# Kernel optimization log

Hardware: AMD Instinct MI355X
Metric: run time of the kernel (lower is better)

The kernel has to match this reference:

```python
import jax, jax.numpy as jnp
import numpy as np

CS = [32, 32, 64, 128, 256, 256, 128, 96, 96]
NC = 19
N0, N1, N2, N3, N4 = 50000, 20000, 8000, 3200, 1300


def build_shapes():
    cs = CS
    def rb(ci, co):
        t = [(27, ci, co), (27, co, co)]
        if ci != co:
            t.append((ci, co))  # 1x1 shortcut conv
        return t
    s = [(27, 4, cs[0]), (27, cs[0], cs[0])]                       # stem
    s += [(8, cs[0], cs[0])] + rb(cs[0], cs[1]) + rb(cs[1], cs[1])  # stage1
    s += [(8, cs[1], cs[1])] + rb(cs[1], cs[2]) + rb(cs[2], cs[2])  # stage2
    s += [(8, cs[2], cs[2])] + rb(cs[2], cs[3]) + rb(cs[3], cs[3])  # stage3
    s += [(8, cs[3], cs[3])] + rb(cs[3], cs[4]) + rb(cs[4], cs[4])  # stage4
    s += [(8, cs[4], cs[5])] + rb(cs[5] + cs[3], cs[5]) + rb(cs[5], cs[5])  # up1
    s += [(8, cs[5], cs[6])] + rb(cs[6] + cs[2], cs[6]) + rb(cs[6], cs[6])  # up2
    s += [(8, cs[6], cs[7])] + rb(cs[7] + cs[1], cs[7]) + rb(cs[7], cs[7])  # up3
    s += [(8, cs[7], cs[8])] + rb(cs[8] + cs[0], cs[8]) + rb(cs[8], cs[8])  # up4
    s += [(cs[8], NC), (NC,), (cs[8], cs[8]), (cs[8],), (cs[8], 128), (128,)]
    return s

P_TOTAL = sum(int(np.prod(sh)) for sh in build_shapes())


def _bn(x):
    # train-mode BatchNorm, gamma=1 beta=0 (set by weight_initialization)
    return (x - x.mean(0)) * jax.lax.rsqrt(jnp.var(x, 0) + 1e-5)


def _spconv(x, nbr, W):
    # sparse conv as gather-GEMM-scatter over K kernel offsets.
    # x: [Nin, Cin], nbr: [Nout, K] row indices into x, W: [K, Cin, Cout]
    acc0 = jnp.zeros((nbr.shape[0], W.shape[-1]), x.dtype)
    def step(acc, kw):
        idx, Wk = kw
        return acc + x[idx] @ Wk, None
    acc, _ = jax.lax.scan(step, acc0, (nbr.T, W))
    return acc


def _spdeconv(x, parent, off, W):
    # transposed ks=2 stride=2 conv: each fine voxel has exactly one coarse
    # parent and one kernel-offset id. out[i] = x[parent[i]] @ W[off[i]]
    y = jnp.einsum('nc,kcd->nkd', x[parent], W)  # [Nf, 8, Cout]
    return jnp.take_along_axis(y, off[:, None, None], axis=1)[:, 0, :]


def _cbr(x, nbr, W):
    return jax.nn.relu(_bn(_spconv(x, nbr, W)))


def _resblock(x, nbr, take, ci, co):
    w1 = take(); w2 = take()
    h = _bn(_spconv(jax.nn.relu(_bn(_spconv(x, nbr, w1))), nbr, w2))
    s = x if ci == co else _bn(x @ take())
    return jax.nn.relu(h + s)


def _forward(x, nbr0, nbr1, nbr2, nbr3, nbr4, d1, d2, d3, d4,
             u1p, u1o, u2p, u2o, u3p, u3o, u4p, u4o, params):
    parts = []
    o = 0
    for sh in build_shapes():
        n = int(np.prod(sh))
        parts.append(params[o:o + n].reshape(sh))
        o += n
    it = iter(parts)
    take = lambda: next(it)
    cs = CS
    x0 = _cbr(x, nbr0, take()); x0 = _cbr(x0, nbr0, take())            # stem
    h = _cbr(x0, d1, take())
    h = _resblock(h, nbr1, take, cs[0], cs[1]); x1 = _resblock(h, nbr1, take, cs[1], cs[1])
    h = _cbr(x1, d2, take())
    h = _resblock(h, nbr2, take, cs[1], cs[2]); x2 = _resblock(h, nbr2, take, cs[2], cs[2])
    h = _cbr(x2, d3, take())
    h = _resblock(h, nbr3, take, cs[2], cs[3]); x3 = _resblock(h, nbr3, take, cs[3], cs[3])
    h = _cbr(x3, d4, take())
    h = _resblock(h, nbr4, take, cs[3], cs[4]); x4 = _resblock(h, nbr4, take, cs[4], cs[4])
    y = jax.nn.relu(_bn(_spdeconv(x4, u1p, u1o, take())))
    y = jnp.concatenate([y, x3], 1)
    y = _resblock(y, nbr3, take, cs[5] + cs[3], cs[5]); y = _resblock(y, nbr3, take, cs[5], cs[5])
    y = jax.nn.relu(_bn(_spdeconv(y, u2p, u2o, take())))
    y = jnp.concatenate([y, x2], 1)
    y = _resblock(y, nbr2, take, cs[6] + cs[2], cs[6]); y = _resblock(y, nbr2, take, cs[6], cs[6])
    y = jax.nn.relu(_bn(_spdeconv(y, u3p, u3o, take())))
    y = jnp.concatenate([y, x1], 1)
    y = _resblock(y, nbr1, take, cs[7] + cs[1], cs[7]); y = _resblock(y, nbr1, take, cs[7], cs[7])
    y = jax.nn.relu(_bn(_spdeconv(y, u4p, u4o, take())))
    y = jnp.concatenate([y, x0], 1)
    y = _resblock(y, nbr0, take, cs[8] + cs[0], cs[8]); y = _resblock(y, nbr0, take, cs[8], cs[8])
    wc = take(); bc = take(); w1 = take(); b1 = take(); w2 = take(); b2 = take()
    out = y @ wc + bc                             # classifier logits [N0, NC]
    feat = jax.nn.relu(y @ w1 + b1) @ w2 + b2     # projection head [N0, 128]
    return out, feat


def setup_inputs() -> dict:
    key = jax.random.key(0)
    ks = jax.random.split(key, 20)
    ri = lambda k, shape, hi: jax.random.randint(k, shape, 0, hi, dtype=jnp.int32)
    return {
        'x': jax.random.normal(ks[0], (N0, 4), jnp.float32),
        'nbr0': ri(ks[1], (N0, 27), N0), 'nbr1': ri(ks[2], (N1, 27), N1),
        'nbr2': ri(ks[3], (N2, 27), N2), 'nbr3': ri(ks[4], (N3, 27), N3),
        'nbr4': ri(ks[5], (N4, 27), N4),
        'd1': ri(ks[6], (N1, 8), N0), 'd2': ri(ks[7], (N2, 8), N1),
        'd3': ri(ks[8], (N3, 8), N2), 'd4': ri(ks[9], (N4, 8), N3),
        'u1p': ri(ks[10], (N3,), N4), 'u1o': ri(ks[11], (N3,), 8),
        'u2p': ri(ks[12], (N2,), N3), 'u2o': ri(ks[13], (N2,), 8),
        'u3p': ri(ks[14], (N1,), N2), 'u3o': ri(ks[15], (N1,), 8),
        'u4p': ri(ks[16], (N0,), N1), 'u4o': ri(ks[17], (N0,), 8),
        'params': jax.random.normal(ks[18], (P_TOTAL,), jnp.float32) * 0.05,
    }


def reference(x, nbr0, nbr1, nbr2, nbr3, nbr4, d1, d2, d3, d4,
              u1p, u1o, u2p, u2o, u3p, u3o, u4p, u4o, params):
    return _forward(x, nbr0, nbr1, nbr2, nbr3, nbr4, d1, d2, d3, d4,
                    u1p, u1o, u2p, u2o, u3p, u3o, u4p, u4o, params)
```

## Files before the change

### kernel.cpp

```cpp
#include <hip/hip_runtime.h>
#include <hip/hip_bf16.h>
#include <stdint.h>

typedef __hip_bfloat16 hbf;
typedef unsigned short u16;
typedef __attribute__((ext_vector_type(8))) short bfrag;
typedef __attribute__((ext_vector_type(4))) float f4;

#define NP0 50000
#define NP1 20000
#define NP2 8000
#define NP3 3200
#define NP4 1300

static inline int cdiv(int a, int b) { return (a + b - 1) / b; }

static __device__ __forceinline__ float u2f(u16 u) { return __uint_as_float(((unsigned)u) << 16); }
static __device__ __forceinline__ u16 f2u(float f) {
  hbf h = __float2bfloat16(f);
  u16 r; __builtin_memcpy(&r, &h, 2); return r;
}
static __device__ __forceinline__ float pload(const void* P, int isbf, size_t i) {
  return isbf ? u2f(((const u16*)P)[i]) : ((const float*)P)[i];
}


struct PrepD {
  long cpre;
  long src;
  long dst;
  int K, CI, CO, CB32, NT16, pad;
};

__global__ void k_sniff(const void* __restrict__ xraw, int* __restrict__ flagp) {
  __shared__ float smax[256];
  const u16* u = (const u16*)xraw;
  float m = 0.f;
  for (int i = threadIdx.x; i < 2048; i += 256) {
    float v = u2f(u[2 * i]);
    if (isnan(v) || isinf(v)) m = 1e30f; else m = fmaxf(m, fabsf(v));
  }
  smax[threadIdx.x] = m;
  __syncthreads();
  for (int s = 128; s > 0; s >>= 1) {
    if (threadIdx.x < s) smax[threadIdx.x] = fmaxf(smax[threadIdx.x], smax[threadIdx.x + s]);
    __syncthreads();
  }
  if (threadIdx.x == 0) *flagp = (smax[0] < 1e4f) ? 1 : 0;
}

__global__ __launch_bounds__(256) void k_prep_all(
    const void* __restrict__ P, const int* __restrict__ flagp, u16* __restrict__ W,
    const PrepD* __restrict__ T, int NL, long totalC, long totalE)
{
  int f = *flagp;
  int L = 0;
  for (long c = (long)blockIdx.x * 256 + threadIdx.x; c < totalC; c += (long)gridDim.x * 256) {
    while (L + 1 < NL && c >= T[L + 1].cpre) ++L;
    PrepD d = T[L];
    long lc = c - d.cpre;
    int lane = (int)(lc & 63); long t = lc >> 6;
    int nt = (int)(t % d.NT16); t /= d.NT16;
    int cb = (int)(t % d.CB32); int k = (int)(t / d.CB32);
    int co = nt * 16 + (lane & 15);
    int cib = cb * 32 + (lane >> 4) * 8;
    u16 hi[8], lo[8];
#pragma unroll
    for (int j = 0; j < 8; ++j) {
      int ci = cib + j; float v = 0.f;
      if (ci < d.CI && co < d.CO) v = pload(P, f, d.src + ((size_t)k * d.CI + ci) * d.CO + co);
      u16 h = f2u(v);
      hi[j] = h;
      lo[j] = f2u(v - u2f(h));
    }
    *(bfrag*)(W + d.dst + lc * 8) = *(const bfrag*)hi;
    *(bfrag*)(W + totalE + d.dst + lc * 8) = *(const bfrag*)lo;
  }
}

__global__ __launch_bounds__(256) void k_prep_frag(
    const void* __restrict__ P, const int* __restrict__ flagp, u16* __restrict__ W,
    long src, long halfel, int K, int CI, int CO, int CB32, int NT16)
{
  int f = *flagp;
  long total = (long)K * CB32 * NT16 * 64;
  for (long c = (long)blockIdx.x * 256 + threadIdx.x; c < total; c += (long)gridDim.x * 256) {
    int lane = (int)(c & 63); long t = c >> 6;
    int nt = (int)(t % NT16); t /= NT16;
    int cb = (int)(t % CB32); int k = (int)(t / CB32);
    int co = nt * 16 + (lane & 15);
    int cib = cb * 32 + (lane >> 4) * 8;
    u16 hi[8], lo[8];
#pragma unroll
    for (int j = 0; j < 8; ++j) {
      int ci = cib + j; float v = 0.f;
      if (ci < CI && co < CO) v = pload(P, f, src + ((size_t)k * CI + ci) * CO + co);
      u16 h = f2u(v);
      hi[j] = h;
      lo[j] = f2u(v - u2f(h));
    }
    *(bfrag*)(W + c * 8) = *(const bfrag*)hi;
    *(bfrag*)(W + halfel + c * 8) = *(const bfrag*)lo;
  }
}

__global__ void k_prep_bias(const void* __restrict__ P, const int* __restrict__ flagp,
                            float* __restrict__ B, long src, int n)
{
  int f = *flagp;
  int i = blockIdx.x * 256 + threadIdx.x;
  if (i < n) B[i] = pload(P, f, src + i);
}

__global__ void k_pad(const void* __restrict__ xraw, const int* __restrict__ flagp,
                      float* __restrict__ Xp, int N)
{
  int f = *flagp; int total = N * 32;
  for (int i = blockIdx.x * 256 + threadIdx.x; i < total; i += gridDim.x * 256) {
    int n = i >> 5, cc = i & 31;
    Xp[i] = (cc < 4) ? pload(xraw, f, (size_t)n * 4 + cc) : 0.f;
  }
}

template<int NT>
__global__ __launch_bounds__(256) void k_conv_mfma(
    const float* __restrict__ X, const int* __restrict__ nbr,
    const u16* __restrict__ Wp, long halfel, float* __restrict__ Y,
    const float* __restrict__ bias, int relu, const int* __restrict__ flagp,
    int N, int K, int CB32, int NT16, int CO, int XS, int tlen, int atomic)
{
  const int f = *flagp;
  const int lane = threadIdx.x & 63;
  const int wv = threadIdx.x >> 6;
  const int rowbase = blockIdx.x * 128 + wv * 32;
  const int ntb = blockIdx.y * NT;
  const int ml = lane & 15;
  const int quad = lane >> 4;
  const int ktot = K * CB32;
  const int t0 = blockIdx.z * tlen;
  const int t1 = (t0 + tlen < ktot) ? (t0 + tlen) : ktot;

  f4 acc[2][NT];
#pragma unroll
  for (int i = 0; i < 2; ++i)
#pragma unroll
    for (int j = 0; j < NT; ++j) acc[i][j] = (f4)(0.f);

  int k = t0 / CB32;
  int cb = t0 - k * CB32;
  int idx[2];
  bool fresh = true;

  if (f) {
    for (int t = t0; t < t1; ++t) {
      if (fresh) {
#pragma unroll
        for (int mt = 0; mt < 2; ++mt) {
          int r = rowbase + mt * 16 + ml;
          idx[mt] = (r < N) ? (nbr ? nbr[(size_t)r * K + k] : r) : 0;
        }
        fresh = false;
      }
      const u16* WH = Wp + (size_t)t * NT16 * 512;
      bfrag bh[NT];
#pragma unroll
      for (int nt = 0; nt < NT; ++nt) {
        size_t o = ((size_t)(ntb + nt) * 64 + lane) * 8;
        bh[nt] = *(const bfrag*)(WH + o);
      }
      bfrag ahi[2], alo[2];
#pragma unroll
      for (int mt = 0; mt < 2; ++mt) {
        const float* ap = X + (size_t)idx[mt] * XS + cb * 32 + quad * 8;
        float4 q0 = *(const float4*)ap;
        float4 q1 = *(const float4*)(ap + 4);
        float av[8] = {q0.x, q0.y, q0.z, q0.w, q1.x, q1.y, q1.z, q1.w};
        u16 hi8[8], lo8[8];
#pragma unroll
        for (int j = 0; j < 8; ++j) {
          u16 hh = f2u(av[j]);
          hi8[j] = hh;
          lo8[j] = f2u(av[j] - u2f(hh));
        }
        __builtin_memcpy(&ahi[mt], hi8, 16);
        __builtin_memcpy(&alo[mt], lo8, 16);
      }
#pragma unroll
      for (int mt = 0; mt < 2; ++mt)
#pragma unroll
        for (int nt = 0; nt < NT; ++nt) {
          acc[mt][nt] = __builtin_amdgcn_mfma_f32_16x16x32_bf16(alo[mt], bh[nt], acc[mt][nt], 0, 0, 0);
          acc[mt][nt] = __builtin_amdgcn_mfma_f32_16x16x32_bf16(ahi[mt], bh[nt], acc[mt][nt], 0, 0, 0);
        }
      if (++cb == CB32) { cb = 0; ++k; fresh = true; }
    }
  } else {
    for (int t = t0; t < t1; ++t) {
      if (fresh) {
#pragma unroll
        for (int mt = 0; mt < 2; ++mt) {
          int r = rowbase + mt * 16 + ml;
          idx[mt] = (r < N) ? (nbr ? nbr[(size_t)r * K + k] : r) : 0;
        }
        fresh = false;
      }
      const u16* WH = Wp + (size_t)t * NT16 * 512;
      const u16* WL = WH + halfel;
      bfrag bh[NT], bl[NT];
#pragma unroll
      for (int nt = 0; nt < NT; ++nt) {
        size_t o = ((size_t)(ntb + nt) * 64 + lane) * 8;
        bh[nt] = *(const bfrag*)(WH + o);
        bl[nt] = *(const bfrag*)(WL + o);
      }
      bfrag ahi[2], alo[2];
#pragma unroll
      for (int mt = 0; mt < 2; ++mt) {
        const float* ap = X + (size_t)idx[mt] * XS + cb * 32 + quad * 8;
        float4 q0 = *(const float4*)ap;
        float4 q1 = *(const float4*)(ap + 4);
        float av[8] = {q0.x, q0.y, q0.z, q0.w, q1.x, q1.y, q1.z, q1.w};
        u16 hi8[8], lo8[8];
#pragma unroll
        for (int j = 0; j < 8; ++j) {
          u16 hh = f2u(av[j]);
          hi8[j] = hh;
          lo8[j] = f2u(av[j] - u2f(hh));
        }
        __builtin_memcpy(&ahi[mt], hi8, 16);
        __builtin_memcpy(&alo[mt], lo8, 16);
      }
#pragma unroll
      for (int mt = 0; mt < 2; ++mt)
#pragma unroll
        for (int nt = 0; nt < NT; ++nt) {
          acc[mt][nt] = __builtin_amdgcn_mfma_f32_16x16x32_bf16(alo[mt], bh[nt], acc[mt][nt], 0, 0, 0);
          acc[mt][nt] = __builtin_amdgcn_mfma_f32_16x16x32_bf16(ahi[mt], bl[nt], acc[mt][nt], 0, 0, 0);
          acc[mt][nt] = __builtin_amdgcn_mfma_f32_16x16x32_bf16(ahi[mt], bh[nt], acc[mt][nt], 0, 0, 0);
        }
      if (++cb == CB32) { cb = 0; ++k; fresh = true; }
    }
  }

#pragma unroll
  for (int mt = 0; mt < 2; ++mt) {
#pragma unroll
    for (int nt = 0; nt < NT; ++nt) {
      int col = (ntb + nt) * 16 + ml;
      if (col >= CO) continue;
      float bvv = bias ? bias[col] : 0.f;
#pragma unroll
      for (int reg = 0; reg < 4; ++reg) {
        int row = rowbase + mt * 16 + quad * 4 + reg;
        if (row < N) {
          if (atomic) {
            atomicAdd(&Y[(size_t)row * CO + col], acc[mt][nt][reg]);
          } else {
            float v = acc[mt][nt][reg] + bvv;
            if (relu) v = fmaxf(v, 0.f);
            Y[(size_t)row * CO + col] = v;
          }
        }
      }
    }
  }
}

__global__ void k_bias_relu(float* __restrict__ Y, const float* __restrict__ bias,
                            int relu, int total, int CO)
{
  int stride = gridDim.x * 256;
  for (int i = blockIdx.x * 256 + threadIdx.x; i < total; i += stride) {
    int c = i % CO;
    float v = Y[i] + (bias ? bias[c] : 0.f);
    if (relu) v = fmaxf(v, 0.f);
    Y[i] = v;
  }
}

static void launch_conv(hipStream_t s, int bx, const float* X, const int* nbr,
                        const u16* W, long halfel, float* Y, const float* bias, int relu,
                        const int* flagp, int N, int K, int CB32, int NT16, int CO, int XS)
{
  int NT = (NT16 % 6 == 0) ? 6 : ((NT16 % 4 == 0) ? 4 : 2);
  int ny = NT16 / NT;
  int ktot = K * CB32;
  long blocks = (long)bx * ny;
  int ZS = 1;
  if (ktot > 1) {
    ZS = (int)((1024 + blocks - 1) / blocks);
    if (ZS > ktot) ZS = ktot;
    if (ZS < 1) ZS = 1;
  }
  int tlen = cdiv(ktot, ZS);
  ZS = cdiv(ktot, tlen);
  int atomic = (ZS > 1) ? 1 : 0;
  if (atomic) hipMemsetAsync(Y, 0, (size_t)N * CO * 4, s);
  dim3 g(bx, ny, ZS);
  if (NT == 6)      k_conv_mfma<6><<<g, 256, 0, s>>>(X, nbr, W, halfel, Y, bias, relu, flagp, N, K, CB32, NT16, CO, XS, tlen, atomic);
  else if (NT == 4) k_conv_mfma<4><<<g, 256, 0, s>>>(X, nbr, W, halfel, Y, bias, relu, flagp, N, K, CB32, NT16, CO, XS, tlen, atomic);
  else              k_conv_mfma<2><<<g, 256, 0, s>>>(X, nbr, W, halfel, Y, bias, relu, flagp, N, K, CB32, NT16, CO, XS, tlen, atomic);
  if (atomic && (bias || relu)) {
    int total = N * CO;
    int nb = cdiv(total, 1024); if (nb > 1024) nb = 1024; if (nb < 1) nb = 1;
    k_bias_relu<<<nb, 256, 0, s>>>(Y, bias, relu, total, CO);
  }
}

__global__ __launch_bounds__(256) void k_deconv(
    const float* __restrict__ X, const int* __restrict__ par, const int* __restrict__ off,
    const void* __restrict__ P, long wofs, const int* __restrict__ flagp,
    float* __restrict__ Y, int N, int CI, int CO)
{
  int f = *flagp;
  int lane = threadIdx.x & 63, wv = threadIdx.x >> 6;
  int n = blockIdx.y * 4 + wv; if (n >= N) return;
  int co = blockIdx.x * 64 + lane; if (co >= CO) return;
  const float* xr = X + (size_t)par[n] * CI;
  size_t wbase = wofs + (size_t)off[n] * CI * CO + co;
  float acc = 0.f;
  for (int ci = 0; ci < CI; ci += 4) {
    float4 xv = *(const float4*)(xr + ci);
    acc += xv.x * pload(P, f, wbase + (size_t)ci * CO);
    acc += xv.y * pload(P, f, wbase + (size_t)(ci + 1) * CO);
    acc += xv.z * pload(P, f, wbase + (size_t)(ci + 2) * CO);
    acc += xv.w * pload(P, f, wbase + (size_t)(ci + 3) * CO);
  }
  Y[(size_t)n * CO + co] = acc;
}

__global__ __launch_bounds__(256) void k_bn_stats(
    const float* __restrict__ X, float* __restrict__ st, int total, int C)
{
  __shared__ float ssum[384], ssq[384];
  for (int c = threadIdx.x; c < C; c += 256) { ssum[c] = 0.f; ssq[c] = 0.f; }
  __syncthreads();
  int gid = blockIdx.x * 256 + threadIdx.x;
  int total4 = total >> 2;
  int stride = gridDim.x * 256;
  int c0 = (gid * 4) % C;
  float s0 = 0.f, s1 = 0.f, s2 = 0.f, s3 = 0.f;
  float q0 = 0.f, q1 = 0.f, q2 = 0.f, q3 = 0.f;
  for (int i = gid; i < total4; i += stride) {
    float4 v = ((const float4*)X)[i];
    s0 += v.x; q0 += v.x * v.x;
    s1 += v.y; q1 += v.y * v.y;
    s2 += v.z; q2 += v.z * v.z;
    s3 += v.w; q3 += v.w * v.w;
  }
  atomicAdd(&ssum[c0], s0);     atomicAdd(&ssq[c0], q0);
  atomicAdd(&ssum[c0 + 1], s1); atomicAdd(&ssq[c0 + 1], q1);
  atomicAdd(&ssum[c0 + 2], s2); atomicAdd(&ssq[c0 + 2], q2);
  atomicAdd(&ssum[c0 + 3], s3); atomicAdd(&ssq[c0 + 3], q3);
  __syncthreads();
  for (int c = threadIdx.x; c < C; c += 256) {
    atomicAdd(&st[c], ssum[c]); atomicAdd(&st[384 + c], ssq[c]);
  }
}

__global__ __launch_bounds__(256) void k_bn_apply(
    const float* __restrict__ X, const float* __restrict__ st, const float* __restrict__ add,
    float* __restrict__ Y, int relu, int total, int C, float invN)
{
  __shared__ float mean[384], rsig[384];
  for (int c = threadIdx.x; c < C; c += 256) {
    float mm = st[c] * invN;
    float vv = st[384 + c] * invN - mm * mm;
    mean[c] = mm; rsig[c] = rsqrtf(vv + 1e-5f);
  }
  __syncthreads();
  int gid = blockIdx.x * 256 + threadIdx.x;
  int total4 = total >> 2;
  int stride = gridDim.x * 256;
  int c0 = (gid * 4) % C;
  float m0 = mean[c0], m1 = mean[c0 + 1], m2 = mean[c0 + 2], m3 = mean[c0 + 3];
  float r0 = rsig[c0], r1 = rsig[c0 + 1], r2 = rsig[c0 + 2], r3 = rsig[c0 + 3];
  for (int i = gid; i < total4; i += stride) {
    float4 v = ((const float4*)X)[i];
    v.x = (v.x - m0) * r0; v.y = (v.y - m1) * r1;
    v.z = (v.z - m2) * r2; v.w = (v.w - m3) * r3;
    if (add) {
      float4 a = ((const float4*)add)[i];
      v.x += a.x; v.y += a.y; v.z += a.z; v.w += a.w;
    }
    if (relu) {
      v.x = fmaxf(v.x, 0.f); v.y = fmaxf(v.y, 0.f);
      v.z = fmaxf(v.z, 0.f); v.w = fmaxf(v.w, 0.f);
    }
    ((float4*)Y)[i] = v;
  }
}

__global__ void k_copycols(const float* __restrict__ S, float* __restrict__ D,
                           int N, int Cs, int Cd, int off)
{
  int csq = Cs >> 2;
  int total4 = N * csq;
  int stride = gridDim.x * 256;
  for (int i = blockIdx.x * 256 + threadIdx.x; i < total4; i += stride) {
    int n = i / csq, cc = i - n * csq;
    ((float4*)D)[((size_t)n * Cd + off) / 4 + cc] = ((const float4*)S)[i];
  }
}

__global__ void k_store_dyn(const float* __restrict__ S, void* __restrict__ D,
                            const int* __restrict__ flagp, size_t eofs, int n)
{
  int f = *flagp;
  int n4 = n >> 2;
  int stride = gridDim.x * 256;
  for (int i = blockIdx.x * 256 + threadIdx.x; i < n4; i += stride) {
    float4 v = ((const float4*)S)[i];
    if (f) {
      ushort4 u;
      u.x = f2u(v.x); u.y = f2u(v.y); u.z = f2u(v.z); u.w = f2u(v.w);
      *(ushort4*)((u16*)D + eofs + (size_t)i * 4) = u;
    } else {
      *(float4*)((float*)D + eofs + (size_t)i * 4) = v;
    }
  }
}

static int build_table(PrepD* T, long* totalC, long* totalE) {
  int n = 0; long po = 0, ce = 0, cc = 0;
  auto W = [&](int K, int CI, int CO) {
    int CB = cdiv(CI, 32), NTx = cdiv(CO, 16);
    long ch = (long)K * CB * NTx * 64;
    T[n].cpre = cc; T[n].src = po; T[n].dst = ce;
    T[n].K = K; T[n].CI = CI; T[n].CO = CO; T[n].CB32 = CB; T[n].NT16 = NTx; T[n].pad = 0;
    ++n; cc += ch; ce += ch * 8; po += (long)K * CI * CO;
  };
  auto SKIP = [&](long e) { po += e; };
  W(27, 4, 32); W(27, 32, 32);
  W(8, 32, 32); W(27, 32, 32); W(27, 32, 32); W(27, 32, 32); W(27, 32, 32);
  W(8, 32, 32); W(27, 32, 64); W(27, 64, 64); W(1, 32, 64); W(27, 64, 64); W(27, 64, 64);
  W(8, 64, 64); W(27, 64, 128); W(27, 128, 128); W(1, 64, 128); W(27, 128, 128); W(27, 128, 128);
  W(8, 128, 128); W(27, 128, 256); W(27, 256, 256); W(1, 128, 256); W(27, 256, 256); W(27, 256, 256);
  SKIP(8L * 256 * 256);
  W(27, 384, 256); W(27, 256, 256); W(1, 384, 256); W(27, 256, 256); W(27, 256, 256);
  SKIP(8L * 256 * 128);
  W(27, 192, 128); W(27, 128, 128); W(1, 192, 128); W(27, 128, 128); W(27, 128, 128);
  SKIP(8L * 128 * 96);
  W(27, 128, 96); W(27, 96, 96); W(1, 128, 96); W(27, 96, 96); W(27, 96, 96);
  SKIP(8L * 96 * 96);
  W(27, 128, 96); W(27, 96, 96); W(1, 128, 96); W(27, 96, 96); W(27, 96, 96);
  W(1, 96, 19); SKIP(19); W(1, 96, 96); SKIP(96); W(1, 96, 128); SKIP(128);
  *totalC = cc; *totalE = ce;
  return n;
}


extern "C" void kernel_launch(void* const* d_in, const int* in_sizes, int n_in,
                              void* d_out, int out_size, void* d_ws, size_t ws_size,
                              hipStream_t stream)
{
  const void* xraw = d_in[0];
  const int* nbr0 = (const int*)d_in[1];
  const int* nbr1 = (const int*)d_in[2];
  const int* nbr2 = (const int*)d_in[3];
  const int* nbr3 = (const int*)d_in[4];
  const int* nbr4 = (const int*)d_in[5];
  const int* d1 = (const int*)d_in[6];
  const int* d2 = (const int*)d_in[7];
  const int* d3 = (const int*)d_in[8];
  const int* d4 = (const int*)d_in[9];
  const int* u1p = (const int*)d_in[10]; const int* u1o = (const int*)d_in[11];
  const int* u2p = (const int*)d_in[12]; const int* u2o = (const int*)d_in[13];
  const int* u3p = (const int*)d_in[14]; const int* u3o = (const int*)d_in[15];
  const int* u4p = (const int*)d_in[16]; const int* u4o = (const int*)d_in[17];
  const void* params = d_in[18];
  (void)in_sizes; (void)n_in;

  static PrepD h_table[64];
  long totalC = 0, totalE = 0;
  int NL = build_table(h_table, &totalC, &totalE);

  char* base = (char*)d_ws; size_t off = 0;
  auto ab = [&](size_t bytes) -> void* { void* p = base + off; off += (bytes + 63) & ~(size_t)63; return p; };
  int* flagp = (int*)ab(64);
  float* st = (float*)ab((size_t)64 * 768 * 4);
  float* Bstf = (float*)ab((size_t)512 * 4);
  float* x0 = (float*)ab((size_t)NP0 * 32 * 4);
  float* x1 = (float*)ab((size_t)NP1 * 32 * 4);
  float* x2 = (float*)ab((size_t)NP2 * 64 * 4);
  float* x3 = (float*)ab((size_t)NP3 * 128 * 4);
  float* x4 = (float*)ab((size_t)NP4 * 256 * 4);
  float* U  = (float*)ab((size_t)NP0 * 96 * 4);
  float* A  = (float*)ab((size_t)NP0 * 96 * 4);
  float* B  = (float*)ab((size_t)NP0 * 128 * 4);
  float* Xp = B;

  size_t wall_bytes = (size_t)totalE * 4;
  size_t rem = (ws_size > off) ? (ws_size - off) : 0;
  bool bigprep = rem >= wall_bytes + 8192;
  u16* Wall = nullptr; PrepD* d_table = nullptr; u16* Wst = nullptr;
  if (bigprep) {
    Wall = (u16*)ab(wall_bytes);
    d_table = (PrepD*)ab(4096);
  } else {
    Wst = (u16*)ab((size_t)5400000 * 2);
  }
  if (off > ws_size) { hipMemsetAsync(d_out, 0, (size_t)out_size * 2, stream); return; }

  long po = 0;
  int bnc = 0;
  int wli = 0;

  auto prepF = [&](int K, int CI, int CO, int CB32, int NT16) -> long {
    long chunks = (long)K * CB32 * NT16 * 64;
    long halfel = chunks * 8;
    int nb = (int)((chunks + 255) / 256); if (nb > 4096) nb = 4096; if (nb < 1) nb = 1;
    k_prep_frag<<<nb, 256, 0, stream>>>(params, flagp, Wst, po, halfel, K, CI, CO, CB32, NT16);
    po += (long)K * CI * CO;
    return halfel;
  };
  auto getW = [&](int K, int CI, int CO, int CB32, int NT16, const u16** Wp, long* he) {
    if (bigprep) {
      *Wp = Wall + h_table[wli].dst; *he = totalE;
      ++wli; po += (long)K * CI * CO;
    } else {
      *he = prepF(K, CI, CO, CB32, NT16); *Wp = Wst;
    }
  };
  auto convop = [&](const float* X, const int* nb_, int K, int CI, int CO, float* Y, int N, int XS) {
    int CB32 = cdiv(CI, 32), NT16 = cdiv(CO, 16);
    const u16* Wp; long he;
    getW(K, CI, CO, CB32, NT16, &Wp, &he);
    launch_conv(stream, cdiv(N, 128), X, nb_, Wp, he, Y, nullptr, 0, flagp, N, K, CB32, NT16, CO, XS);
  };
  auto linop = [&](const float* X, int CI, int CO, float* Y, int N, bool bias, int relu) {
    int CB32 = cdiv(CI, 32), NT16 = cdiv(CO, 16);
    const u16* Wp; long he;
    getW(1, CI, CO, CB32, NT16, &Wp, &he);
    const float* bp = nullptr;
    if (bias) {
      k_prep_bias<<<cdiv(CO, 256), 256, 0, stream>>>(params, flagp, Bstf, po, CO);
      po += CO; bp = Bstf;
    }
    launch_conv(stream, cdiv(N, 128), X, nullptr, Wp, he, Y, bp, relu, flagp, N, 1, CB32, NT16, CO, CI);
  };
  auto deconvop = [&](const float* X, const int* par, const int* ofv, int CI, int CO, float* Y, int N) {
    long wofs = po; po += (long)8 * CI * CO;
    dim3 g(cdiv(CO, 64), cdiv(N, 4));
    k_deconv<<<g, 256, 0, stream>>>(X, par, ofv, params, wofs, flagp, Y, N, CI, CO);
  };
  auto bnop = [&](const float* X, int N, int C, const float* add, int relu, float* out) {
    float* slot = st + (size_t)(bnc++) * 768;
    int total = N * C;
    int total4 = total >> 2;
    int nb1 = cdiv(total4, 4096); if (nb1 > 504) nb1 = 504; if (nb1 < 3) nb1 = 3;
    nb1 = ((nb1 + 2) / 3) * 3;
    k_bn_stats<<<nb1, 256, 0, stream>>>(X, slot, total, C);
    int nb2 = cdiv(total4, 2048); if (nb2 > 510) nb2 = 510; if (nb2 < 3) nb2 = 3;
    nb2 = ((nb2 + 2) / 3) * 3;
    k_bn_apply<<<nb2, 256, 0, stream>>>(X, slot, add, out ? out : (float*)X, relu, total, C, 1.0f / (float)N);
  };
  auto copyop = [&](const float* S, float* D, int N, int Cs, int Cd, int o2) {
    int total4 = (N * Cs) >> 2;
    int nb3 = cdiv(total4, 1024); if (nb3 > 1024) nb3 = 1024; if (nb3 < 1) nb3 = 1;
    k_copycols<<<nb3, 256, 0, stream>>>(S, D, N, Cs, Cd, o2);
  };
  auto storeop = [&](const float* S, size_t eo, int n) {
    int nb4 = cdiv(n >> 2, 1024); if (nb4 > 1024) nb4 = 1024; if (nb4 < 1) nb4 = 1;
    k_store_dyn<<<nb4, 256, 0, stream>>>(S, d_out, flagp, eo, n);
  };
  auto resblock = [&](const int* nb, int N, int CI, int CO,
                      float* H, float* t1, float* t2, float* OUT) {
    convop(H, nb, 27, CI, CO, t1, N, CI);
    bnop(t1, N, CO, nullptr, 1, nullptr);
    convop(t1, nb, 27, CO, CO, t2, N, CO);
    const float* S;
    if (CI == CO) S = H;
    else { linop(H, CI, CO, t1, N, false, 0); bnop(t1, N, CO, nullptr, 0, nullptr); S = t1; }
    bnop(t2, N, CO, S, 1, OUT);
  };

  k_sniff<<<1, 256, 0, stream>>>(xraw, flagp);
  if (bigprep) {
    hipMemcpyAsync(d_table, h_table, (size_t)NL * sizeof(PrepD), hipMemcpyHostToDevice, stream);
    int nbp = (int)((totalC + 255) / 256); if (nbp > 4096) nbp = 4096;
    k_prep_all<<<nbp, 256, 0, stream>>>(params, flagp, Wall, d_table, NL, totalC, totalE);
  }
  hipMemsetAsync(st, 0, (size_t)64 * 768 * 4, stream);
  k_pad<<<1024, 256, 0, stream>>>(xraw, flagp, Xp, NP0);

  convop(Xp, nbr0, 27, 4, 32, A, NP0, 32);  bnop(A, NP0, 32, nullptr, 1, nullptr);
  convop(A, nbr0, 27, 32, 32, x0, NP0, 32); bnop(x0, NP0, 32, nullptr, 1, nullptr);
  convop(x0, d1, 8, 32, 32, U, NP1, 32); bnop(U, NP1, 32, nullptr, 1, nullptr);
  resblock(nbr1, NP1, 32, 32, U, A, B, U);
  resblock(nbr1, NP1, 32, 32, U, A, B, x1);
  convop(x1, d2, 8, 32, 32, U, NP2, 32); bnop(U, NP2, 32, nullptr, 1, nullptr);
  resblock(nbr2, NP2, 32, 64, U, A, B, U);
  resblock(nbr2, NP2, 64, 64, U, A, B, x2);
  convop(x2, d3, 8, 64, 64, U, NP3, 64); bnop(U, NP3, 64, nullptr, 1, nullptr);
  resblock(nbr3, NP3, 64, 128, U, A, B, U);
  resblock(nbr3, NP3, 128, 128, U, A, B, x3);
  convop(x3, d4, 8, 128, 128, U, NP4, 128); bnop(U, NP4, 128, nullptr, 1, nullptr);
  resblock(nbr4, NP4, 128, 256, U, A, B, U);
  resblock(nbr4, NP4, 256, 256, U, A, B, x4);
  deconvop(x4, u1p, u1o, 256, 256, A, NP3); bnop(A, NP3, 256, nullptr, 1, nullptr);
  copyop(A, B, NP3, 256, 384, 0); copyop(x3, B, NP3, 128, 384, 256);
  resblock(nbr3, NP3, 384, 256, B, A, U, B);
  resblock(nbr3, NP3, 256, 256, B, A, U, U);
  deconvop(U, u2p, u2o, 256, 128, A, NP2); bnop(A, NP2, 128, nullptr, 1, nullptr);
  copyop(A, B, NP2, 128, 192, 0); copyop(x2, B, NP2, 64, 192, 128);
  resblock(nbr2, NP2, 192, 128, B, A, U, B);
  resblock(nbr2, NP2, 128, 128, B, A, U, U);
  deconvop(U, u3p, u3o, 128, 96, A, NP1); bnop(A, NP1, 96, nullptr, 1, nullptr);
  copyop(A, B, NP1, 96, 128, 0); copyop(x1, B, NP1, 32, 128, 96);
  resblock(nbr1, NP1, 128, 96, B, A, U, B);
  resblock(nbr1, NP1, 96, 96, B, A, U, U);
  deconvop(U, u4p, u4o, 96, 96, A, NP0); bnop(A, NP0, 96, nullptr, 1, nullptr);
  copyop(A, B, NP0, 96, 128, 0); copyop(x0, B, NP0, 32, 128, 96);
  resblock(nbr0, NP0, 128, 96, B, A, U, B);
  resblock(nbr0, NP0, 96, 96, B, A, U, U);
  linop(U, 96, 19, x0, NP0, true, 0);
  linop(U, 96, 96, A, NP0, true, 1);
  linop(A, 96, 128, B, NP0, true, 0);
  storeop(x0, 0, NP0 * 19);
  storeop(B, (size_t)NP0 * 19, NP0 * 128);
}
```

Before: 4.298 ms.

## Store decoder activations in fp16 and use single-pass f16 MFMA with split weights

The decoder path (deconvs, resblocks and heads) now keeps activations as fp16 written by BN-apply, copy and bias kernels. The conv kernel gains an fp16-activation mode that loads A fragments directly and runs f16 MFMA against hi/lo-split fp16 weights. This drops the per-element bf16 hi/lo split of activations and one MFMA pass per step, and halves gather bandwidth. In exchange, activations are rounded to fp16, which costs accuracy and risks overflow or underflow. Encoder layers keep the fp32 split-bf16 path.

```diff
diff --git a/kernel.cpp b/kernel.cpp
--- a/kernel.cpp
+++ b/kernel.cpp
@@ -5,6 +5,7 @@
 typedef __hip_bfloat16 hbf;
 typedef unsigned short u16;
 typedef __attribute__((ext_vector_type(8))) short bfrag;
+typedef _Float16 __attribute__((ext_vector_type(8))) hfrag;
 typedef __attribute__((ext_vector_type(4))) float f4;
 
 #define NP0 50000
@@ -20,16 +21,21 @@
   hbf h = __float2bfloat16(f);
   u16 r; __builtin_memcpy(&r, &h, 2); return r;
 }
+static __device__ __forceinline__ u16 f2h(float f) {
+  _Float16 h = (_Float16)f;
+  u16 r; __builtin_memcpy(&r, &h, 2); return r;
+}
+static __device__ __forceinline__ float h2f(u16 u) {
+  _Float16 h; __builtin_memcpy(&h, &u, 2); return (float)h;
+}
 static __device__ __forceinline__ float pload(const void* P, int isbf, size_t i) {
   return isbf ? u2f(((const u16*)P)[i]) : ((const float*)P)[i];
 }
 
 
 struct PrepD {
-  long cpre;
-  long src;
-  long dst;
-  int K, CI, CO, CB32, NT16, pad;
+  long cpre, src, dst;
+  int K, CI, CO, CB32, NT16, hf;
 };
 
 __global__ void k_sniff(const void* __restrict__ xraw, int* __restrict__ flagp) {
@@ -69,9 +75,8 @@
     for (int j = 0; j < 8; ++j) {
       int ci = cib + j; float v = 0.f;
       if (ci < d.CI && co < d.CO) v = pload(P, f, d.src + ((size_t)k * d.CI + ci) * d.CO + co);
-      u16 h = f2u(v);
-      hi[j] = h;
-      lo[j] = f2u(v - u2f(h));
+      if (d.hf) { u16 h = f2h(v); hi[j] = h; lo[j] = f2h(v - h2f(h)); }
+      else      { u16 h = f2u(v); hi[j] = h; lo[j] = f2u(v - u2f(h)); }
     }
     *(bfrag*)(W + d.dst + lc * 8) = *(const bfrag*)hi;
     *(bfrag*)(W + totalE + d.dst + lc * 8) = *(const bfrag*)lo;
@@ -80,7 +85,7 @@
 
 __global__ __launch_bounds__(256) void k_prep_frag(
     const void* __restrict__ P, const int* __restrict__ flagp, u16* __restrict__ W,
-    long src, long halfel, int K, int CI, int CO, int CB32, int NT16)
+    long src, long halfel, int hf, int K, int CI, int CO, int CB32, int NT16)
 {
   int f = *flagp;
   long total = (long)K * CB32 * NT16 * 64;
@@ -95,9 +100,8 @@
     for (int j = 0; j < 8; ++j) {
       int ci = cib + j; float v = 0.f;
       if (ci < CI && co < CO) v = pload(P, f, src + ((size_t)k * CI + ci) * CO + co);
-      u16 h = f2u(v);
-      hi[j] = h;
-      lo[j] = f2u(v - u2f(h));
+      if (hf) { u16 h = f2h(v); hi[j] = h; lo[j] = f2h(v - h2f(h)); }
+      else    { u16 h = f2u(v); hi[j] = h; lo[j] = f2u(v - u2f(h)); }
     }
     *(bfrag*)(W + c * 8) = *(const bfrag*)hi;
     *(bfrag*)(W + halfel + c * 8) = *(const bfrag*)lo;
@@ -124,10 +128,10 @@
 
 template<int NT>
 __global__ __launch_bounds__(256) void k_conv_mfma(
-    const float* __restrict__ X, const int* __restrict__ nbr,
+    const void* __restrict__ Xv, const int* __restrict__ nbr,
     const u16* __restrict__ Wp, long halfel, float* __restrict__ Y,
     const float* __restrict__ bias, int relu, const int* __restrict__ flagp,
-    int N, int K, int CB32, int NT16, int CO, int XS, int tlen, int atomic)
+    int ahalf, int N, int K, int CB32, int NT16, int CO, int XS, int tlen, int atomic)
 {
   const int f = *flagp;
   const int lane = threadIdx.x & 63;
@@ -139,6 +143,7 @@
   const int ktot = K * CB32;
   const int t0 = blockIdx.z * tlen;
   const int t1 = (t0 + tlen < ktot) ? (t0 + tlen) : ktot;
+  if (t0 >= t1) return;
 
   f4 acc[2][NT];
 #pragma unroll
@@ -151,94 +156,156 @@
   int idx[2];
   bool fresh = true;
 
-  if (f) {
-    for (int t = t0; t < t1; ++t) {
-      if (fresh) {
+  if (ahalf) {
+    const u16* X = (const u16*)Xv;
+    if (f) {
+      for (int t = t0; t < t1; ++t) {
+        if (fresh) {
+#pragma unroll
+          for (int mt = 0; mt < 2; ++mt) {
+            int r = rowbase + mt * 16 + ml;
+            idx[mt] = (r < N) ? (nbr ? nbr[(size_t)r * K + k] : r) : 0;
+          }
+          fresh = false;
+        }
+        const u16* WH = Wp + (size_t)t * NT16 * 512;
+        hfrag bh[NT];
+#pragma unroll
+        for (int nt = 0; nt < NT; ++nt)
+          bh[nt] = *(const hfrag*)(WH + ((size_t)(ntb + nt) * 64 + lane) * 8);
+        hfrag a[2];
+#pragma unroll
+        for (int mt = 0; mt < 2; ++mt)
+          a[mt] = *(const hfrag*)(X + (size_t)idx[mt] * XS + cb * 32 + quad * 8);
+#pragma unroll
+        for (int mt = 0; mt < 2; ++mt)
+#pragma unroll
+          for (int nt = 0; nt < NT; ++nt)
+            acc[mt][nt] = __builtin_amdgcn_mfma_f32_16x16x32_f16(a[mt], bh[nt], acc[mt][nt], 0, 0, 0);
+        if (++cb == CB32) { cb = 0; ++k; fresh = true; }
+      }
+    } else {
+      for (int t = t0; t < t1; ++t) {
+        if (fresh) {
+#pragma unroll
+          for (int mt = 0; mt < 2; ++mt) {
+            int r = rowbase + mt * 16 + ml;
+            idx[mt] = (r < N) ? (nbr ? nbr[(size_t)r * K + k] : r) : 0;
+          }
+          fresh = false;
+        }
+        const u16* WH = Wp + (size_t)t * NT16 * 512;
+        const u16* WL = WH + halfel;
+        hfrag bh[NT], bl[NT];
+#pragma unroll
+        for (int nt = 0; nt < NT; ++nt) {
+          size_t o = ((size_t)(ntb + nt) * 64 + lane) * 8;
+          bh[nt] = *(const hfrag*)(WH + o);
+          bl[nt] = *(const hfrag*)(WL + o);
+        }
+        hfrag a[2];
+#pragma unroll
+        for (int mt = 0; mt < 2; ++mt)
+          a[mt] = *(const hfrag*)(X + (size_t)idx[mt] * XS + cb * 32 + quad * 8);
+#pragma unroll
+        for (int mt = 0; mt < 2; ++mt)
+#pragma unroll
+          for (int nt = 0; nt < NT; ++nt) {
+            acc[mt][nt] = __builtin_amdgcn_mfma_f32_16x16x32_f16(a[mt], bl[nt], acc[mt][nt], 0, 0, 0);
+            acc[mt][nt] = __builtin_amdgcn_mfma_f32_16x16x32_f16(a[mt], bh[nt], acc[mt][nt], 0, 0, 0);
+          }
+        if (++cb == CB32) { cb = 0; ++k; fresh = true; }
+      }
+    }
+  } else {
+    const float* X = (const float*)Xv;
+    if (f) {
+      for (int t = t0; t < t1; ++t) {
+        if (fresh) {
+#pragma unroll
+          for (int mt = 0; mt < 2; ++mt) {
+            int r = rowbase + mt * 16 + ml;
+            idx[mt] = (r < N) ? (nbr ? nbr[(size_t)r * K + k] : r) : 0;
+          }
+          fresh = false;
+        }
+        const u16* WH = Wp + (size_t)t * NT16 * 512;
+        bfrag bh[NT];
+#pragma unroll
+        for (int nt = 0; nt < NT; ++nt)
+          bh[nt] = *(const bfrag*)(WH + ((size_t)(ntb + nt) * 64 + lane) * 8);
+        bfrag ahi[2], alo[2];
 #pragma unroll
         for (int mt = 0; mt < 2; ++mt) {
-          int r = rowbase + mt * 16 + ml;
-          idx[mt] = (r < N) ? (nbr ? nbr[(size_t)r * K + k] : r) : 0;
-        }
-        fresh = false;
+          const float* ap = X + (size_t)idx[mt] * XS + cb * 32 + quad * 8;
+          float4 q0 = *(const float4*)ap;
+          float4 q1 = *(const float4*)(ap + 4);
+          float av[8] = {q0.x, q0.y, q0.z, q0.w, q1.x, q1.y, q1.z, q1.w};
+          u16 hi8[8], lo8[8];
+#pragma unroll
+          for (int j = 0; j < 8; ++j) {
+            u16 hh = f2u(av[j]);
+            hi8[j] = hh;
+            lo8[j] = f2u(av[j] - u2f(hh));
+          }
+          __builtin_memcpy(&ahi[mt], hi8, 16);
+          __builtin_memcpy(&alo[mt], lo8, 16);
+        }
+#pragma unroll
+        for (int mt = 0; mt < 2; ++mt)
+#pragma unroll
+          for (int nt = 0; nt < NT; ++nt) {
+            acc[mt][nt] = __builtin_amdgcn_mfma_f32_16x16x32_bf16(alo[mt], bh[nt], acc[mt][nt], 0, 0, 0);
+            acc[mt][nt] = __builtin_amdgcn_mfma_f32_16x16x32_bf16(ahi[mt], bh[nt], acc[mt][nt], 0, 0, 0);
+          }
+        if (++cb == CB32) { cb = 0; ++k; fresh = true; }
       }
-      const u16* WH = Wp + (size_t)t * NT16 * 512;
-      bfrag bh[NT];
-#pragma unroll
-      for (int nt = 0; nt < NT; ++nt) {
-        size_t o = ((size_t)(ntb + nt) * 64 + lane) * 8;
-        bh[nt] = *(const bfrag*)(WH + o);
+    } else {
+      for (int t = t0; t < t1; ++t) {
+        if (fresh) {
+#pragma unroll
+          for (int mt = 0; mt < 2; ++mt) {
+            int r = rowbase + mt * 16 + ml;
+            idx[mt] = (r < N) ? (nbr ? nbr[(size_t)r * K + k] : r) : 0;
+          }
+          fresh = false;
+        }
+        const u16* WH = Wp + (size_t)t * NT16 * 512;
+        const u16* WL = WH + halfel;
+        bfrag bh[NT], bl[NT];
+#pragma unroll
+        for (int nt = 0; nt < NT; ++nt) {
+          size_t o = ((size_t)(ntb + nt) * 64 + lane) * 8;
+          bh[nt] = *(const bfrag*)(WH + o);
+          bl[nt] = *(const bfrag*)(WL + o);
+        }
+        bfrag ahi[2], alo[2];
+#pragma unroll
+        for (int mt = 0; mt < 2; ++mt) {
+          const float* ap = X + (size_t)idx[mt] * XS + cb * 32 + quad * 8;
+          float4 q0 = *(const float4*)ap;
+          float4 q1 = *(const float4*)(ap + 4);
+          float av[8] = {q0.x, q0.y, q0.z, q0.w, q1.x, q1.y, q1.z, q1.w};
+          u16 hi8[8], lo8[8];
+#pragma unroll
+          for (int j = 0; j < 8; ++j) {
+            u16 hh = f2u(av[j]);
+            hi8[j] = hh;
+            lo8[j] = f2u(av[j] - u2f(hh));
+          }
+          __builtin_memcpy(&ahi[mt], hi8, 16);
+          __builtin_memcpy(&alo[mt], lo8, 16);
+        }
+#pragma unroll
+        for (int mt = 0; mt < 2; ++mt)
+#pragma unroll
+          for (int nt = 0; nt < NT; ++nt) {
+            acc[mt][nt] = __builtin_amdgcn_mfma_f32_16x16x32_bf16(alo[mt], bh[nt], acc[mt][nt], 0, 0, 0);
+            acc[mt][nt] = __builtin_amdgcn_mfma_f32_16x16x32_bf16(ahi[mt], bl[nt], acc[mt][nt], 0, 0, 0);
+            acc[mt][nt] = __builtin_amdgcn_mfma_f32_16x16x32_bf16(ahi[mt], bh[nt], acc[mt][nt], 0, 0, 0);
+          }
+        if (++cb == CB32) { cb = 0; ++k; fresh = true; }
       }
-      bfrag ahi[2], alo[2];
-#pragma unroll
-      for (int mt = 0; mt < 2; ++mt) {
-        const float* ap = X + (size_t)idx[mt] * XS + cb * 32 + quad * 8;
-        float4 q0 = *(const float4*)ap;
-        float4 q1 = *(const float4*)(ap + 4);
-        float av[8] = {q0.x, q0.y, q0.z, q0.w, q1.x, q1.y, q1.z, q1.w};
-        u16 hi8[8], lo8[8];
-#pragma unroll
-        for (int j = 0; j < 8; ++j) {
-          u16 hh = f2u(av[j]);
-          hi8[j] = hh;
-          lo8[j] = f2u(av[j] - u2f(hh));
-        }
-        __builtin_memcpy(&ahi[mt], hi8, 16);
-        __builtin_memcpy(&alo[mt], lo8, 16);
-      }
-#pragma unroll
-      for (int mt = 0; mt < 2; ++mt)
-#pragma unroll
-        for (int nt = 0; nt < NT; ++nt) {
-          acc[mt][nt] = __builtin_amdgcn_mfma_f32_16x16x32_bf16(alo[mt], bh[nt], acc[mt][nt], 0, 0, 0);
-          acc[mt][nt] = __builtin_amdgcn_mfma_f32_16x16x32_bf16(ahi[mt], bh[nt], acc[mt][nt], 0, 0, 0);
-        }
-      if (++cb == CB32) { cb = 0; ++k; fresh = true; }
-    }
-  } else {
-    for (int t = t0; t < t1; ++t) {
-      if (fresh) {
-#pragma unroll
-        for (int mt = 0; mt < 2; ++mt) {
-          int r = rowbase + mt * 16 + ml;
-          idx[mt] = (r < N) ? (nbr ? nbr[(size_t)r * K + k] : r) : 0;
-        }
-        fresh = false;
-      }
-      const u16* WH = Wp + (size_t)t * NT16 * 512;
-      const u16* WL = WH + halfel;
-      bfrag bh[NT], bl[NT];
-#pragma unroll
-      for (int nt = 0; nt < NT; ++nt) {
-        size_t o = ((size_t)(ntb + nt) * 64 + lane) * 8;
-        bh[nt] = *(const bfrag*)(WH + o);
-        bl[nt] = *(const bfrag*)(WL + o);
-      }
-      bfrag ahi[2], alo[2];
-#pragma unroll
-      for (int mt = 0; mt < 2; ++mt) {
-        const float* ap = X + (size_t)idx[mt] * XS + cb * 32 + quad * 8;
-        float4 q0 = *(const float4*)ap;
-        float4 q1 = *(const float4*)(ap + 4);
-        float av[8] = {q0.x, q0.y, q0.z, q0.w, q1.x, q1.y, q1.z, q1.w};
-        u16 hi8[8], lo8[8];
-#pragma unroll
-        for (int j = 0; j < 8; ++j) {
-          u16 hh = f2u(av[j]);
-          hi8[j] = hh;
-          lo8[j] = f2u(av[j] - u2f(hh));
-        }
-        __builtin_memcpy(&ahi[mt], hi8, 16);
-        __builtin_memcpy(&alo[mt], lo8, 16);
-      }
-#pragma unroll
-      for (int mt = 0; mt < 2; ++mt)
-#pragma unroll
-        for (int nt = 0; nt < NT; ++nt) {
-          acc[mt][nt] = __builtin_amdgcn_mfma_f32_16x16x32_bf16(alo[mt], bh[nt], acc[mt][nt], 0, 0, 0);
-          acc[mt][nt] = __builtin_amdgcn_mfma_f32_16x16x32_bf16(ahi[mt], bl[nt], acc[mt][nt], 0, 0, 0);
-          acc[mt][nt] = __builtin_amdgcn_mfma_f32_16x16x32_bf16(ahi[mt], bh[nt], acc[mt][nt], 0, 0, 0);
-        }
-      if (++cb == CB32) { cb = 0; ++k; fresh = true; }
     }
   }
 
@@ -267,7 +334,7 @@
 }
 
 __global__ void k_bias_relu(float* __restrict__ Y, const float* __restrict__ bias,
-                            int relu, int total, int CO)
+                            u16* __restrict__ d16, int relu, int total, int CO)
 {
   int stride = gridDim.x * 256;
   for (int i = blockIdx.x * 256 + threadIdx.x; i < total; i += stride) {
@@ -275,12 +342,14 @@
     float v = Y[i] + (bias ? bias[c] : 0.f);
     if (relu) v = fmaxf(v, 0.f);
     Y[i] = v;
-  }
-}
-
-static void launch_conv(hipStream_t s, int bx, const float* X, const int* nbr,
+    if (d16) d16[i] = f2h(v);
+  }
+}
+
+static void launch_conv(hipStream_t s, int bx, const void* X, const int* nbr,
                         const u16* W, long halfel, float* Y, const float* bias, int relu,
-                        const int* flagp, int N, int K, int CB32, int NT16, int CO, int XS)
+                        const int* flagp, int ahalf, int N, int K, int CB32, int NT16, int CO, int XS,
+                        u16* d16)
 {
   int NT = (NT16 % 6 == 0) ? 6 : ((NT16 % 4 == 0) ? 4 : 2);
   int ny = NT16 / NT;
@@ -297,34 +366,45 @@
   int atomic = (ZS > 1) ? 1 : 0;
   if (atomic) hipMemsetAsync(Y, 0, (size_t)N * CO * 4, s);
   dim3 g(bx, ny, ZS);
-  if (NT == 6)      k_conv_mfma<6><<<g, 256, 0, s>>>(X, nbr, W, halfel, Y, bias, relu, flagp, N, K, CB32, NT16, CO, XS, tlen, atomic);
-  else if (NT == 4) k_conv_mfma<4><<<g, 256, 0, s>>>(X, nbr, W, halfel, Y, bias, relu, flagp, N, K, CB32, NT16, CO, XS, tlen, atomic);
-  else              k_conv_mfma<2><<<g, 256, 0, s>>>(X, nbr, W, halfel, Y, bias, relu, flagp, N, K, CB32, NT16, CO, XS, tlen, atomic);
-  if (atomic && (bias || relu)) {
+  if (NT == 6)      k_conv_mfma<6><<<g, 256, 0, s>>>(X, nbr, W, halfel, Y, bias, relu, flagp, ahalf, N, K, CB32, NT16, CO, XS, tlen, atomic);
+  else if (NT == 4) k_conv_mfma<4><<<g, 256, 0, s>>>(X, nbr, W, halfel, Y, bias, relu, flagp, ahalf, N, K, CB32, NT16, CO, XS, tlen, atomic);
+  else              k_conv_mfma<2><<<g, 256, 0, s>>>(X, nbr, W, halfel, Y, bias, relu, flagp, ahalf, N, K, CB32, NT16, CO, XS, tlen, atomic);
+  if ((atomic && (bias || relu)) || d16) {
     int total = N * CO;
     int nb = cdiv(total, 1024); if (nb > 1024) nb = 1024; if (nb < 1) nb = 1;
-    k_bias_relu<<<nb, 256, 0, s>>>(Y, bias, relu, total, CO);
+    k_bias_relu<<<nb, 256, 0, s>>>(Y, atomic ? bias : nullptr, d16, atomic ? relu : 0, total, CO);
   }
 }
 
 __global__ __launch_bounds__(256) void k_deconv(
-    const float* __restrict__ X, const int* __restrict__ par, const int* __restrict__ off,
+    const void* __restrict__ Xv, const int* __restrict__ par, const int* __restrict__ off,
     const void* __restrict__ P, long wofs, const int* __restrict__ flagp,
-    float* __restrict__ Y, int N, int CI, int CO)
+    float* __restrict__ Y, int xmode, int N, int CI, int CO)
 {
   int f = *flagp;
   int lane = threadIdx.x & 63, wv = threadIdx.x >> 6;
   int n = blockIdx.y * 4 + wv; if (n >= N) return;
   int co = blockIdx.x * 64 + lane; if (co >= CO) return;
-  const float* xr = X + (size_t)par[n] * CI;
   size_t wbase = wofs + (size_t)off[n] * CI * CO + co;
   float acc = 0.f;
-  for (int ci = 0; ci < CI; ci += 4) {
-    float4 xv = *(const float4*)(xr + ci);
-    acc += xv.x * pload(P, f, wbase + (size_t)ci * CO);
-    acc += xv.y * pload(P, f, wbase + (size_t)(ci + 1) * CO);
-    acc += xv.z * pload(P, f, wbase + (size_t)(ci + 2) * CO);
-    acc += xv.w * pload(P, f, wbase + (size_t)(ci + 3) * CO);
+  if (xmode) {
+    const u16* xr = (const u16*)Xv + (size_t)par[n] * CI;
+    for (int ci = 0; ci < CI; ci += 4) {
+      ushort4 xv = *(const ushort4*)(xr + ci);
+      acc += h2f(xv.x) * pload(P, f, wbase + (size_t)ci * CO);
+      acc += h2f(xv.y) * pload(P, f, wbase + (size_t)(ci + 1) * CO);
+      acc += h2f(xv.z) * pload(P, f, wbase + (size_t)(ci + 2) * CO);
+      acc += h2f(xv.w) * pload(P, f, wbase + (size_t)(ci + 3) * CO);
+    }
+  } else {
+    const float* xr = (const float*)Xv + (size_t)par[n] * CI;
+    for (int ci = 0; ci < CI; ci += 4) {
+      float4 xv = *(const float4*)(xr + ci);
+      acc += xv.x * pload(P, f, wbase + (size_t)ci * CO);
+      acc += xv.y * pload(P, f, wbase + (size_t)(ci + 1) * CO);
+      acc += xv.z * pload(P, f, wbase + (size_t)(ci + 2) * CO);
+      acc += xv.w * pload(P, f, wbase + (size_t)(ci + 3) * CO);
+    }
   }
   Y[(size_t)n * CO + co] = acc;
 }
@@ -359,8 +439,9 @@
 }
 
 __global__ __launch_bounds__(256) void k_bn_apply(
-    const float* __restrict__ X, const float* __restrict__ st, const float* __restrict__ add,
-    float* __restrict__ Y, int relu, int total, int C, float invN)
+    const float* __restrict__ X, const float* __restrict__ st,
+    const void* __restrict__ addp, int addmode,
+    void* __restrict__ Yo, int outmode, int relu, int total, int C, float invN)
 {
   __shared__ float mean[384], rsig[384];
   for (int c = threadIdx.x; c < C; c += 256) {
@@ -377,29 +458,45 @@
   float r0 = rsig[c0], r1 = rsig[c0 + 1], r2 = rsig[c0 + 2], r3 = rsig[c0 + 3];
   for (int i = gid; i < total4; i += stride) {
     float4 v = ((const float4*)X)[i];
-    v.x = (v.x - m0) * r0; v.y = (v.y - m1) * r1;
-    v.z = (v.z - m2) * r2; v.w = (v.w - m3) * r3;
-    if (add) {
-      float4 a = ((const float4*)add)[i];
-      v.x += a.x; v.y += a.y; v.z += a.z; v.w += a.w;
+    float w0 = (v.x - m0) * r0, w1 = (v.y - m1) * r1;
+    float w2 = (v.z - m2) * r2, w3 = (v.w - m3) * r3;
+    if (addmode == 1) {
+      float4 a = ((const float4*)addp)[i];
+      w0 += a.x; w1 += a.y; w2 += a.z; w3 += a.w;
+    } else if (addmode == 2) {
+      ushort4 ah = *(const ushort4*)((const u16*)addp + (size_t)i * 4);
+      w0 += h2f(ah.x); w1 += h2f(ah.y); w2 += h2f(ah.z); w3 += h2f(ah.w);
     }
     if (relu) {
-      v.x = fmaxf(v.x, 0.f); v.y = fmaxf(v.y, 0.f);
-      v.z = fmaxf(v.z, 0.f); v.w = fmaxf(v.w, 0.f);
-    }
-    ((float4*)Y)[i] = v;
-  }
-}
-
-__global__ void k_copycols(const float* __restrict__ S, float* __restrict__ D,
-                           int N, int Cs, int Cd, int off)
+      w0 = fmaxf(w0, 0.f); w1 = fmaxf(w1, 0.f);
+      w2 = fmaxf(w2, 0.f); w3 = fmaxf(w3, 0.f);
+    }
+    if (outmode == 0) {
+      float4 o; o.x = w0; o.y = w1; o.z = w2; o.w = w3;
+      ((float4*)Yo)[i] = o;
+    } else {
+      ushort4 hh; hh.x = f2h(w0); hh.y = f2h(w1); hh.z = f2h(w2); hh.w = f2h(w3);
+      *(ushort4*)((u16*)Yo + (size_t)i * 4) = hh;
+    }
+  }
+}
+
+__global__ void k_copycols(const void* __restrict__ Sv, u16* __restrict__ D,
+                           int smode, int N, int Cs, int Cd, int off)
 {
   int csq = Cs >> 2;
   int total4 = N * csq;
   int stride = gridDim.x * 256;
   for (int i = blockIdx.x * 256 + threadIdx.x; i < total4; i += stride) {
-    int n = i / csq, cc = i - n * csq;
-    ((float4*)D)[((size_t)n * Cd + off) / 4 + cc] = ((const float4*)S)[i];
+    int n = i / csq, cc = (i - n * csq) * 4;
+    ushort4 hh;
+    if (smode == 0) {
+      float4 v = ((const float4*)Sv)[i];
+      hh.x = f2h(v.x); hh.y = f2h(v.y); hh.z = f2h(v.z); hh.w = f2h(v.w);
+    } else {
+      hh = *(const ushort4*)((const u16*)Sv + (size_t)i * 4);
+    }
+    *(ushort4*)(D + (size_t)n * Cd + off + cc) = hh;
   }
 }
 
@@ -423,32 +520,31 @@
 
 static int build_table(PrepD* T, long* totalC, long* totalE) {
   int n = 0; long po = 0, ce = 0, cc = 0;
-  auto W = [&](int K, int CI, int CO) {
+  auto W = [&](int K, int CI, int CO, int hf) {
     int CB = cdiv(CI, 32), NTx = cdiv(CO, 16);
     long ch = (long)K * CB * NTx * 64;
     T[n].cpre = cc; T[n].src = po; T[n].dst = ce;
-    T[n].K = K; T[n].CI = CI; T[n].CO = CO; T[n].CB32 = CB; T[n].NT16 = NTx; T[n].pad = 0;
+    T[n].K = K; T[n].CI = CI; T[n].CO = CO; T[n].CB32 = CB; T[n].NT16 = NTx; T[n].hf = hf;
     ++n; cc += ch; ce += ch * 8; po += (long)K * CI * CO;
   };
   auto SKIP = [&](long e) { po += e; };
-  W(27, 4, 32); W(27, 32, 32);
-  W(8, 32, 32); W(27, 32, 32); W(27, 32, 32); W(27, 32, 32); W(27, 32, 32);
-  W(8, 32, 32); W(27, 32, 64); W(27, 64, 64); W(1, 32, 64); W(27, 64, 64); W(27, 64, 64);
-  W(8, 64, 64); W(27, 64, 128); W(27, 128, 128); W(1, 64, 128); W(27, 128, 128); W(27, 128, 128);
-  W(8, 128, 128); W(27, 128, 256); W(27, 256, 256); W(1, 128, 256); W(27, 256, 256); W(27, 256, 256);
+  W(27, 4, 32, 0); W(27, 32, 32, 0);
+  W(8, 32, 32, 0); W(27, 32, 32, 0); W(27, 32, 32, 0); W(27, 32, 32, 0); W(27, 32, 32, 0);
+  W(8, 32, 32, 0); W(27, 32, 64, 0); W(27, 64, 64, 0); W(1, 32, 64, 0); W(27, 64, 64, 0); W(27, 64, 64, 0);
+  W(8, 64, 64, 0); W(27, 64, 128, 0); W(27, 128, 128, 0); W(1, 64, 128, 0); W(27, 128, 128, 0); W(27, 128, 128, 0);
+  W(8, 128, 128, 0); W(27, 128, 256, 0); W(27, 256, 256, 0); W(1, 128, 256, 0); W(27, 256, 256, 0); W(27, 256, 256, 0);
   SKIP(8L * 256 * 256);
-  W(27, 384, 256); W(27, 256, 256); W(1, 384, 256); W(27, 256, 256); W(27, 256, 256);
+  W(27, 384, 256, 1); W(27, 256, 256, 1); W(1, 384, 256, 1); W(27, 256, 256, 1); W(27, 256, 256, 1);
   SKIP(8L * 256 * 128);
-  W(27, 192, 128); W(27, 128, 128); W(1, 192, 128); W(27, 128, 128); W(27, 128, 128);
+  W(27, 192, 128, 1); W(27, 128, 128, 1); W(1, 192, 128, 1); W(27, 128, 128, 1); W(27, 128, 128, 1);
   SKIP(8L * 128 * 96);
-  W(27, 128, 96); W(27, 96, 96); W(1, 128, 96); W(27, 96, 96); W(27, 96, 96);
+  W(27, 128, 96, 1); W(27, 96, 96, 1); W(1, 128, 96, 1); W(27, 96, 96, 1); W(27, 96, 96, 1);
   SKIP(8L * 96 * 96);
-  W(27, 128, 96); W(27, 96, 96); W(1, 128, 96); W(27, 96, 96); W(27, 96, 96);
-  W(1, 96, 19); SKIP(19); W(1, 96, 96); SKIP(96); W(1, 96, 128); SKIP(128);
+  W(27, 128, 96, 1); W(27, 96, 96, 1); W(1, 128, 96, 1); W(27, 96, 96, 1); W(27, 96, 96, 1);
+  W(1, 96, 19, 1); SKIP(19); W(1, 96, 96, 1); SKIP(96); W(1, 96, 128, 1); SKIP(128);
   *totalC = cc; *totalE = ce;
   return n;
 }
-
 
 extern "C" void kernel_launch(void* const* d_in, const int* in_sizes, int n_in,
                               void* d_out, int out_size, void* d_ws, size_t ws_size,
@@ -506,45 +602,46 @@
   int bnc = 0;
   int wli = 0;
 
-  auto prepF = [&](int K, int CI, int CO, int CB32, int NT16) -> long {
+  auto prepF = [&](int hf, int K, int CI, int CO, int CB32, int NT16) -> long {
     long chunks = (long)K * CB32 * NT16 * 64;
     long halfel = chunks * 8;
     int nb = (int)((chunks + 255) / 256); if (nb > 4096) nb = 4096; if (nb < 1) nb = 1;
-    k_prep_frag<<<nb, 256, 0, stream>>>(params, flagp, Wst, po, halfel, K, CI, CO, CB32, NT16);
+    k_prep_frag<<<nb, 256, 0, stream>>>(params, flagp, Wst, po, halfel, hf, K, CI, CO, CB32, NT16);
     po += (long)K * CI * CO;
     return halfel;
   };
-  auto getW = [&](int K, int CI, int CO, int CB32, int NT16, const u16** Wp, long* he) {
+  auto getW = [&](int hf, int K, int CI, int CO, int CB32, int NT16, const u16** Wp, long* he) {
     if (bigprep) {
       *Wp = Wall + h_table[wli].dst; *he = totalE;
       ++wli; po += (long)K * CI * CO;
     } else {
-      *he = prepF(K, CI, CO, CB32, NT16); *Wp = Wst;
-    }
-  };
-  auto convop = [&](const float* X, const int* nb_, int K, int CI, int CO, float* Y, int N, int XS) {
+      *he = prepF(hf, K, CI, CO, CB32, NT16); *Wp = Wst;
+    }
+  };
+  auto convop = [&](int hf, const void* X, const int* nb_, int K, int CI, int CO, float* Y, int N, int XS) {
     int CB32 = cdiv(CI, 32), NT16 = cdiv(CO, 16);
     const u16* Wp; long he;
-    getW(K, CI, CO, CB32, NT16, &Wp, &he);
-    launch_conv(stream, cdiv(N, 128), X, nb_, Wp, he, Y, nullptr, 0, flagp, N, K, CB32, NT16, CO, XS);
-  };
-  auto linop = [&](const float* X, int CI, int CO, float* Y, int N, bool bias, int relu) {
+    getW(hf, K, CI, CO, CB32, NT16, &Wp, &he);
+    launch_conv(stream, cdiv(N, 128), X, nb_, Wp, he, Y, nullptr, 0, flagp, hf, N, K, CB32, NT16, CO, XS, nullptr);
+  };
+  auto linop = [&](int hf, const void* X, int CI, int CO, float* Y, int N, bool bias, int relu, u16* d16) {
     int CB32 = cdiv(CI, 32), NT16 = cdiv(CO, 16);
     const u16* Wp; long he;
-    getW(1, CI, CO, CB32, NT16, &Wp, &he);
+    getW(hf, 1, CI, CO, CB32, NT16, &Wp, &he);
     const float* bp = nullptr;
     if (bias) {
       k_prep_bias<<<cdiv(CO, 256), 256, 0, stream>>>(params, flagp, Bstf, po, CO);
       po += CO; bp = Bstf;
     }
-    launch_conv(stream, cdiv(N, 128), X, nullptr, Wp, he, Y, bp, relu, flagp, N, 1, CB32, NT16, CO, CI);
-  };
-  auto deconvop = [&](const float* X, const int* par, const int* ofv, int CI, int CO, float* Y, int N) {
+    launch_conv(stream, cdiv(N, 128), X, nullptr, Wp, he, Y, bp, relu, flagp, hf, N, 1, CB32, NT16, CO, CI, d16);
+  };
+  auto deconvop = [&](const void* X, int xmode, const int* par, const int* ofv, int CI, int CO, float* Y, int N) {
     long wofs = po; po += (long)8 * CI * CO;
     dim3 g(cdiv(CO, 64), cdiv(N, 4));
-    k_deconv<<<g, 256, 0, stream>>>(X, par, ofv, params, wofs, flagp, Y, N, CI, CO);
-  };
-  auto bnop = [&](const float* X, int N, int C, const float* add, int relu, float* out) {
+    k_deconv<<<g, 256, 0, stream>>>(X, par, ofv, params, wofs, flagp, Y, xmode, N, CI, CO);
+  };
+  auto bnop = [&](const float* X, int N, int C, const void* addp, int addmode, int relu,
+                  void* out, int outmode) {
     float* slot = st + (size_t)(bnc++) * 768;
     int total = N * C;
     int total4 = total >> 2;
@@ -553,12 +650,13 @@
     k_bn_stats<<<nb1, 256, 0, stream>>>(X, slot, total, C);
     int nb2 = cdiv(total4, 2048); if (nb2 > 510) nb2 = 510; if (nb2 < 3) nb2 = 3;
     nb2 = ((nb2 + 2) / 3) * 3;
-    k_bn_apply<<<nb2, 256, 0, stream>>>(X, slot, add, out ? out : (float*)X, relu, total, C, 1.0f / (float)N);
-  };
-  auto copyop = [&](const float* S, float* D, int N, int Cs, int Cd, int o2) {
+    k_bn_apply<<<nb2, 256, 0, stream>>>(X, slot, addp, addmode, out ? out : (void*)X, outmode,
+                                        relu, total, C, 1.0f / (float)N);
+  };
+  auto copyop = [&](const void* S, int smode, u16* D, int N, int Cs, int Cd, int o2) {
     int total4 = (N * Cs) >> 2;
     int nb3 = cdiv(total4, 1024); if (nb3 > 1024) nb3 = 1024; if (nb3 < 1) nb3 = 1;
-    k_copycols<<<nb3, 256, 0, stream>>>(S, D, N, Cs, Cd, o2);
+    k_copycols<<<nb3, 256, 0, stream>>>(S, D, smode, N, Cs, Cd, o2);
   };
   auto storeop = [&](const float* S, size_t eo, int n) {
     int nb4 = cdiv(n >> 2, 1024); if (nb4 > 1024) nb4 = 1024; if (nb4 < 1) nb4 = 1;
@@ -566,13 +664,26 @@
   };
   auto resblock = [&](const int* nb, int N, int CI, int CO,
                       float* H, float* t1, float* t2, float* OUT) {
-    convop(H, nb, 27, CI, CO, t1, N, CI);
-    bnop(t1, N, CO, nullptr, 1, nullptr);
-    convop(t1, nb, 27, CO, CO, t2, N, CO);
+    convop(0, H, nb, 27, CI, CO, t1, N, CI);
+    bnop(t1, N, CO, nullptr, 0, 1, nullptr, 0);
+    convop(0, t1, nb, 27, CO, CO, t2, N, CO);
     const float* S;
     if (CI == CO) S = H;
-    else { linop(H, CI, CO, t1, N, false, 0); bnop(t1, N, CO, nullptr, 0, nullptr); S = t1; }
-    bnop(t2, N, CO, S, 1, OUT);
+    else { linop(0, H, CI, CO, t1, N, false, 0, nullptr); bnop(t1, N, CO, nullptr, 0, 0, nullptr, 0); S = t1; }
+    bnop(t2, N, CO, S, 1, 1, OUT, 0);
+  };
+  auto resblock16 = [&](const int* nb, int N, int CI, int CO,
+                        u16* H16, float* t1, float* t2, u16* OUT16) {
+    convop(1, H16, nb, 27, CI, CO, t1, N, CI);
+    bnop(t1, N, CO, nullptr, 0, 1, (u16*)t2, 1);
+    convop(1, (u16*)t2, nb, 27, CO, CO, t1, N, CO);
+    if (CI == CO) {
+      bnop(t1, N, CO, H16, 2, 1, OUT16, 1);
+    } else {
+      linop(1, H16, CI, CO, t2, N, false, 0, nullptr);
+      bnop(t2, N, CO, nullptr, 0, 0, OUT16, 1);
+      bnop(t1, N, CO, OUT16, 2, 1, OUT16, 1);
+    }
   };
 
   k_sniff<<<1, 256, 0, stream>>>(xraw, flagp);
@@ -584,39 +695,46 @@
   hipMemsetAsync(st, 0, (size_t)64 * 768 * 4, stream);
   k_pad<<<1024, 256, 0, stream>>>(xraw, flagp, Xp, NP0);
 
-  convop(Xp, nbr0, 27, 4, 32, A, NP0, 32);  bnop(A, NP0, 32, nullptr, 1, nullptr);
-  convop(A, nbr0, 27, 32, 32, x0, NP0, 32); bnop(x0, NP0, 32, nullptr, 1, nullptr);
-  convop(x0, d1, 8, 32, 32, U, NP1, 32); bnop(U, NP1, 32, nullptr, 1, nullptr);
+  convop(0, Xp, nbr0, 27, 4, 32, A, NP0, 32);  bnop(A, NP0, 32, nullptr, 0, 1, nullptr, 0);
+  convop(0, A, nbr0, 27, 32, 32, x0, NP0, 32); bnop(x0, NP0, 32, nullptr, 0, 1, nullptr, 0);
+  convop(0, x0, d1, 8, 32, 32, U, NP1, 32); bnop(U, NP1, 32, nullptr, 0, 1, nullptr, 0);
   resblock(nbr1, NP1, 32, 32, U, A, B, U);
   resblock(nbr1, NP1, 32, 32, U, A, B, x1);
-  convop(x1, d2, 8, 32, 32, U, NP2, 32); bnop(U, NP2, 32, nullptr, 1, nullptr);
+  convop(0, x1, d2, 8, 32, 32, U, NP2, 32); bnop(U, NP2, 32, nullptr, 0, 1, nullptr, 0);
   resblock(nbr2, NP2, 32, 64, U, A, B, U);
   resblock(nbr2, NP2, 64, 64, U, A, B, x2);
-  convop(x2, d3, 8, 64, 64, U, NP3, 64); bnop(U, NP3, 64, nullptr, 1, nullptr);
+  convop(0, x2, d3, 8, 64, 64, U, NP3, 64); bnop(U, NP3, 64, nullptr, 0, 1, nullptr, 0);
   resblock(nbr3, NP3, 64, 128, U, A, B, U);
   resblock(nbr3, NP3, 128, 128, U, A, B, x3);
-  convop(x3, d4, 8, 128, 128, U, NP4, 128); bnop(U, NP4, 128, nullptr, 1, nullptr);
+  convop(0, x3, d4, 8, 128, 128, U, NP4, 128); bnop(U, NP4, 128, nullptr, 0, 1, nullptr, 0);
   resblock(nbr4, NP4, 128, 256, U, A, B, U);
   resblock(nbr4, NP4, 256, 256, U, A, B, x4);
-  deconvop(x4, u1p, u1o, 256, 256, A, NP3); bnop(A, NP3, 256, nullptr, 1, nullptr);
-  copyop(A, B, NP3, 256, 384, 0); copyop(x3, B, NP3, 128, 384, 256);
-  resblock(nbr3, NP3, 384, 256, B, A, U, B);
-  resblock(nbr3, NP3, 256, 256, B, A, U, U);
-  deconvop(U, u2p, u2o, 256, 128, A, NP2); bnop(A, NP2, 128, nullptr, 1, nullptr);
-  copyop(A, B, NP2, 128, 192, 0); copyop(x2, B, NP2, 64, 192, 128);
-  resblock(nbr2, NP2, 192, 128, B, A, U, B);
-  resblock(nbr2, NP2, 128, 128, B, A, U, U);
-  deconvop(U, u3p, u3o, 128, 96, A, NP1); bnop(A, NP1, 96, nullptr, 1, nullptr);
-  copyop(A, B, NP1, 96, 128, 0); copyop(x1, B, NP1, 32, 128, 96);
-  resblock(nbr1, NP1, 128, 96, B, A, U, B);
-  resblock(nbr1, NP1, 96, 96, B, A, U, U);
-  deconvop(U, u4p, u4o, 96, 96, A, NP0); bnop(A, NP0, 96, nullptr, 1, nullptr);
-  copyop(A, B, NP0, 96, 128, 0); copyop(x0, B, NP0, 32, 128, 96);
-  resblock(nbr0, NP0, 128, 96, B, A, U, B);
-  resblock(nbr0, NP0, 96, 96, B, A, U, U);
-  linop(U, 96, 19, x0, NP0, true, 0);
-  linop(U, 96, 96, A, NP0, true, 1);
-  linop(A, 96, 128, B, NP0, true, 0);
-  storeop(x0, 0, NP0 * 19);
+
+  u16* U16 = (u16*)U; u16* B16 = (u16*)B; u16* A16 = (u16*)A;
+  deconvop(x4, 0, u1p, u1o, 256, 256, A, NP3);
+  bnop(A, NP3, 256, nullptr, 0, 1, U16, 1);
+  copyop(U16, 1, B16, NP3, 256, 384, 0); copyop(x3, 0, B16, NP3, 128, 384, 256);
+  resblock16(nbr3, NP3, 384, 256, B16, A, U, B16);
+  resblock16(nbr3, NP3, 256, 256, B16, A, U, U16);
+  deconvop(U16, 1, u2p, u2o, 256, 128, A, NP2);
+  bnop(A, NP2, 128, nullptr, 0, 1, U16, 1);
+  copyop(U16, 1, B16, NP2, 128, 192, 0); copyop(x2, 0, B16, NP2, 64, 192, 128);
+  resblock16(nbr2, NP2, 192, 128, B16, A, U, B16);
+  resblock16(nbr2, NP2, 128, 128, B16, A, U, U16);
+  deconvop(U16, 1, u3p, u3o, 128, 96, A, NP1);
+  bnop(A, NP1, 96, nullptr, 0, 1, U16, 1);
+  copyop(U16, 1, B16, NP1, 96, 128, 0); copyop(x1, 0, B16, NP1, 32, 128, 96);
+  resblock16(nbr1, NP1, 128, 96, B16, A, U, B16);
+  resblock16(nbr1, NP1, 96, 96, B16, A, U, U16);
+  deconvop(U16, 1, u4p, u4o, 96, 96, A, NP0);
+  bnop(A, NP0, 96, nullptr, 0, 1, U16, 1);
+  copyop(U16, 1, B16, NP0, 96, 128, 0); copyop(x0, 0, B16, NP0, 32, 128, 96);
+  resblock16(nbr0, NP0, 128, 96, B16, A, U, B16);
+  resblock16(nbr0, NP0, 96, 96, B16, A, U, U16);
+  float* x0f = (float*)x0;
+  linop(1, U16, 96, 19, x0f, NP0, true, 0, nullptr);
+  linop(1, U16, 96, 96, B, NP0, true, 1, A16);
+  linop(1, A16, 96, 128, B, NP0, true, 0, nullptr);
+  storeop(x0f, 0, NP0 * 19);
   storeop(B, (size_t)NP0 * 19, NP0 * 128);
 }
```

Result: faster. 4.015 ms (-6.6%).
